# Kernel tuning notes

Measured on AMD Instinct MI355X. Metric: run time of the kernel, lower is better.

## Reference

```python
import jax, jax.numpy as jnp
import numpy as np

BITS = 4
MAXQ = 15            # 2**BITS - 1
PACK = 32 // BITS    # 8 int4 values per int32
GROUPSIZE = 128
M, K, N = 2048, 4096, 4096
G = K // GROUPSIZE


def setup_inputs() -> dict:
    key = jax.random.key(0)
    k1, k2, k3, k4, k5 = jax.random.split(key, 5)
    x = jax.random.normal(k1, (M, K), dtype=jnp.float32)
    qweight = jax.random.randint(k2, (K // PACK, N), 0, 2147483647, dtype=jnp.int32)
    qzeros = jax.random.randint(k3, (G, N // PACK), 0, 2147483647, dtype=jnp.int32)
    scales = jax.random.uniform(k4, (G, N), dtype=jnp.float32) * 0.01
    g_idx = (jnp.arange(K, dtype=jnp.int32) // GROUPSIZE).astype(jnp.int32)
    bias = jax.random.normal(k5, (N,), dtype=jnp.float32)
    return {"x": x, "qweight": qweight, "qzeros": qzeros,
            "scales": scales, "g_idx": g_idx, "bias": bias}


def _dequantize(qweight, qzeros, scales, g_idx):
    shifts = (jnp.arange(PACK, dtype=jnp.int32) * BITS)
    # unpack weights along K: [K//8, N] -> [K//8, 8, N] -> [K, N]
    w_int = ((qweight[:, None, :] >> shifts[None, :, None]) & MAXQ)
    w_int = w_int.reshape(K, N)
    # unpack zeros along N: [G, N//8] -> [G, N//8, 8] -> [G, N]; kernel adds 1
    z_int = ((qzeros[:, :, None] >> shifts[None, None, :]) & MAXQ) + 1
    z_int = z_int.reshape(G, N)
    # group-wise dequant: W[k, n] = (w - zeros[g_idx[k]]) * scales[g_idx[k]]
    W = (w_int - z_int[g_idx]).astype(jnp.float32) * scales[g_idx]
    return W  # [K, N]


def reference(x, qweight, qzeros, scales, g_idx, bias):
    W = _dequantize(qweight, qzeros, scales, g_idx)
    return x @ W + bias  # [M, N]
```

## Files before the change

kernel.cpp:

```cpp
#include <hip/hip_runtime.h>
#include <hip/hip_bf16.h>
#include <stdint.h>

#define M_DIM 2048
#define K_DIM 4096
#define N_DIM 4096

typedef __attribute__((ext_vector_type(8))) short short8;
typedef __attribute__((ext_vector_type(4))) float f32x4;

__device__ __forceinline__ uint32_t bf16pk(float a, float b) {
  uint32_t ua = __float_as_uint(a);
  ua = (ua + 0x7FFFu + ((ua >> 16) & 1u)) >> 16;
  uint32_t ub = __float_as_uint(b);
  ub = (ub + 0x7FFFu + ((ub >> 16) & 1u)) >> 16;
  return ua | (ub << 16);
}

__global__ void __launch_bounds__(256) cvt_x_kernel(const float* __restrict__ x,
                                                    uint32_t* __restrict__ xImg) {
  int bid = blockIdx.x;
  int mt = bid >> 6;
  int kt = bid & 63;
  int tid = threadIdx.x;
  uint32_t* tileOut = xImg + (size_t)(mt * 64 + kt) * 4096;
  const float* xbase = x + (size_t)mt * 128 * K_DIM + kt * 64;
#pragma unroll
  for (int i = 0; i < 4; ++i) {
    int o = i * 256 + tid;
    int m = o >> 3;
    int slot = o & 7;
    int k8 = slot ^ (m & 7);
    const float* src = xbase + (size_t)m * K_DIM + k8 * 8;
    float4 f0 = *(const float4*)(src);
    float4 f1 = *(const float4*)(src + 4);
    uint4 pk;
    pk.x = bf16pk(f0.x, f0.y);
    pk.y = bf16pk(f0.z, f0.w);
    pk.z = bf16pk(f1.x, f1.y);
    pk.w = bf16pk(f1.z, f1.w);
    *(uint4*)(tileOut + (size_t)o * 4) = pk;
  }
}

__global__ void __launch_bounds__(256) deq_w_kernel(const uint32_t* __restrict__ qweight,
                                                    const uint32_t* __restrict__ qzeros,
                                                    const float* __restrict__ scales,
                                                    uint32_t* __restrict__ wImg) {
  __shared__ uint32_t img[4096];
  int bid = blockIdx.x;
  int kt = bid & 63;
  int nt = bid >> 6;
  int tid = threadIdx.x;
  int n = tid & 127;
  int kh = tid >> 7;
  int g = kt >> 1;
  int gn = nt * 128 + n;

  uint32_t zq = qzeros[g * (N_DIM / 8) + (gn >> 3)];
  int z = (int)((zq >> ((gn & 7) * 4)) & 15u) + 1;
  float s = scales[g * N_DIM + gn];

#pragma unroll
  for (int j = 0; j < 4; ++j) {
    int k8 = kh * 4 + j;
    uint32_t q = qweight[(size_t)(kt * 8 + k8) * N_DIM + gn];
    float f[8];
#pragma unroll
    for (int v = 0; v < 8; ++v) {
      int w = (int)((q >> (4 * v)) & 15u);
      f[v] = (float)(w - z) * s;
    }
    uint4 pk;
    pk.x = bf16pk(f[0], f[1]);
    pk.y = bf16pk(f[2], f[3]);
    pk.z = bf16pk(f[4], f[5]);
    pk.w = bf16pk(f[6], f[7]);
    int slot = k8 ^ (n & 7);
    *(uint4*)(&img[(n * 8 + slot) * 4]) = pk;
  }
  __syncthreads();
  uint32_t* tileOut = wImg + (size_t)(nt * 64 + kt) * 4096;
#pragma unroll
  for (int i = 0; i < 4; ++i) {
    int o = i * 256 + tid;
    *(uint4*)(tileOut + (size_t)o * 4) = *(const uint4*)(&img[o * 4]);
  }
}

__global__ void __launch_bounds__(256) gemm_kernel(const uint32_t* __restrict__ xImg,
                                                   const uint32_t* __restrict__ wImg,
                                                   const float* __restrict__ bias,
                                                   float* __restrict__ out) {
  __shared__ uint32_t sA[4096];
  __shared__ uint32_t sB[4096];
  int bid = blockIdx.x;
  int nb = bid & 31;
  int mb = bid >> 5;
  int tid = threadIdx.x;
  int lane = tid & 63;
  int wid = tid >> 6;
  int wr = wid >> 1, wc = wid & 1;
  int lr = lane & 15, lk = lane >> 4;

  f32x4 acc[4][4];
#pragma unroll
  for (int i = 0; i < 4; ++i)
#pragma unroll
    for (int j = 0; j < 4; ++j) acc[i][j] = f32x4{0.f, 0.f, 0.f, 0.f};

  const char* aTile = (const char*)(xImg + (size_t)mb * 64 * 4096);
  const char* bTile = (const char*)(wImg + (size_t)nb * 64 * 4096);

  int swz = (lr & 7) << 4;
  int rowA[4], rowB[4];
#pragma unroll
  for (int i = 0; i < 4; ++i) rowA[i] = (wr * 64 + i * 16 + lr) * 128;
#pragma unroll
  for (int j = 0; j < 4; ++j) rowB[j] = (wc * 64 + j * 16 + lr) * 128;

  for (int kt = 0; kt < 64; ++kt) {
#pragma unroll
    for (int s2 = 0; s2 < 4; ++s2) {
      int c = wid * 4 + s2;
      int off = c * 1024 + lane * 16;
      __builtin_amdgcn_global_load_lds(
          (__attribute__((address_space(1))) void*)(aTile + off),
          (__attribute__((address_space(3))) void*)((char*)sA + c * 1024), 16, 0, 0);
      __builtin_amdgcn_global_load_lds(
          (__attribute__((address_space(1))) void*)(bTile + off),
          (__attribute__((address_space(3))) void*)((char*)sB + c * 1024), 16, 0, 0);
    }
    __syncthreads();
#pragma unroll
    for (int ks = 0; ks < 2; ++ks) {
      int kb = ks * 64 + lk * 16;
      int ko = kb ^ swz;
      short8 af[4], bf[4];
#pragma unroll
      for (int i = 0; i < 4; ++i)
        af[i] = *(const short8*)((const char*)sA + rowA[i] + ko);
#pragma unroll
      for (int j = 0; j < 4; ++j)
        bf[j] = *(const short8*)((const char*)sB + rowB[j] + ko);
#pragma unroll
      for (int i = 0; i < 4; ++i)
#pragma unroll
        for (int j = 0; j < 4; ++j)
          acc[i][j] = __builtin_amdgcn_mfma_f32_16x16x32_bf16(af[i], bf[j], acc[i][j], 0, 0, 0);
    }
    __syncthreads();
    aTile += 16384;
    bTile += 16384;
  }

  int colBase = nb * 128 + wc * 64 + lr;
  int rowBase = mb * 128 + wr * 64 + lk * 4;
#pragma unroll
  for (int j = 0; j < 4; ++j) {
    int col = colBase + j * 16;
    float bj = bias[col];
#pragma unroll
    for (int i = 0; i < 4; ++i) {
      int row = rowBase + i * 16;
#pragma unroll
      for (int r = 0; r < 4; ++r) {
        out[(size_t)(row + r) * N_DIM + col] = acc[i][j][r] + bj;
      }
    }
  }
}

__global__ void fallback_kernel(const float* __restrict__ x, const uint32_t* __restrict__ qweight,
                                const uint32_t* __restrict__ qzeros, const float* __restrict__ scales,
                                const float* __restrict__ bias, float* __restrict__ out) {
  __shared__ float xs[16][17];
  __shared__ float ws[16][17];
  int tx = threadIdx.x, ty = threadIdx.y;
  int col = blockIdx.x * 16 + tx;
  int row = blockIdx.y * 16 + ty;
  float acc = 0.f;
  for (int k0 = 0; k0 < K_DIM; k0 += 16) {
    xs[ty][tx] = x[(size_t)row * K_DIM + k0 + tx];
    int k = k0 + ty;
    int g = k >> 7;
    uint32_t q = qweight[(size_t)(k >> 3) * N_DIM + col];
    int w = (int)((q >> ((k & 7) * 4)) & 15u);
    uint32_t zq = qzeros[g * (N_DIM / 8) + (col >> 3)];
    int z = (int)((zq >> ((col & 7) * 4)) & 15u) + 1;
    ws[ty][tx] = (float)(w - z) * scales[g * N_DIM + col];
    __syncthreads();
#pragma unroll
    for (int kk = 0; kk < 16; ++kk) acc += xs[ty][kk] * ws[kk][tx];
    __syncthreads();
  }
  out[(size_t)row * N_DIM + col] = acc + bias[col];
}

extern "C" void kernel_launch(void* const* d_in, const int* in_sizes, int n_in,
                              void* d_out, int out_size, void* d_ws, size_t ws_size,
                              hipStream_t stream) {
  const float* x = (const float*)d_in[0];
  const uint32_t* qweight = (const uint32_t*)d_in[1];
  const uint32_t* qzeros = (const uint32_t*)d_in[2];
  const float* scales = (const float*)d_in[3];
  const float* bias = (const float*)d_in[5];
  float* out = (float*)d_out;

  const size_t X_IMG_BYTES = (size_t)16 * 64 * 16384;
  const size_t W_IMG_BYTES = (size_t)32 * 64 * 16384;

  if (ws_size >= X_IMG_BYTES + W_IMG_BYTES) {
    uint32_t* xImg = (uint32_t*)d_ws;
    uint32_t* wImg = (uint32_t*)((char*)d_ws + X_IMG_BYTES);
    cvt_x_kernel<<<1024, 256, 0, stream>>>(x, xImg);
    deq_w_kernel<<<2048, 256, 0, stream>>>(qweight, qzeros, scales, wImg);
    gemm_kernel<<<512, 256, 0, stream>>>(xImg, wImg, bias, out);
  } else {
    fallback_kernel<<<dim3(N_DIM / 16, M_DIM / 16), dim3(16, 16), 0, stream>>>(
        x, qweight, qzeros, scales, bias, out);
  }
}
```

Baseline: 97.92 us.

## Restructure GEMM into 128x256 tiles with triple-buffered LDS prefetch pipeline

The GEMM now runs 512-thread blocks, each computing a 128x256 output tile, so every A tile is reused across two N tiles. LDS is triple buffered (three 48 KB stages), and global-to-LDS loads for tile t+2 are interleaved with MFMA phases. Synchronisation uses explicit barriers, vmcnt waits and s_setprio around the MFMA groups. The aim is to hide load latency and cut the redundant A traffic. In exchange, 144 KB of LDS and launch_bounds(512,2) may limit occupancy, and the grid shrinks to 256 blocks.

```diff
diff --git a/kernel.cpp b/kernel.cpp
--- a/kernel.cpp
+++ b/kernel.cpp
@@ -88,20 +88,27 @@
   }
 }
 
-__global__ void __launch_bounds__(256) gemm_kernel(const uint32_t* __restrict__ xImg,
-                                                   const uint32_t* __restrict__ wImg,
-                                                   const float* __restrict__ bias,
-                                                   float* __restrict__ out) {
-  __shared__ uint32_t sA[4096];
-  __shared__ uint32_t sB[4096];
-  int bid = blockIdx.x;
-  int nb = bid & 31;
-  int mb = bid >> 5;
-  int tid = threadIdx.x;
-  int lane = tid & 63;
-  int wid = tid >> 6;
-  int wr = wid >> 1, wc = wid & 1;
-  int lr = lane & 15, lk = lane >> 4;
+__device__ __forceinline__ void glds16(const char* g, char* l) {
+  __builtin_amdgcn_global_load_lds((__attribute__((address_space(1))) void*)g,
+                                   (__attribute__((address_space(3))) void*)l, 16, 0, 0);
+}
+__device__ __forceinline__ void stage16k(const char* src, char* dst, int tid, int wid) {
+  glds16(src + tid * 16,        dst + wid * 1024);
+  glds16(src + 8192 + tid * 16, dst + 8192 + wid * 1024);
+}
+
+__global__ void __launch_bounds__(512, 2) gemm_kernel(const uint32_t* __restrict__ xImg,
+                                                      const uint32_t* __restrict__ wImg,
+                                                      const float* __restrict__ bias,
+                                                      float* __restrict__ out) {
+  __shared__ uint4 ldsv[9216];
+  char* lds = (char*)ldsv;
+  const int tid = threadIdx.x;
+  const int lane = tid & 63, wid = tid >> 6;
+  const int wr = wid >> 2, wc = wid & 3;
+  const int lr = lane & 15, lk = lane >> 4;
+  const int bid = blockIdx.x;
+  const int nbp = bid & 15, mb = bid >> 4;
 
   f32x4 acc[4][4];
 #pragma unroll
@@ -109,53 +116,104 @@
 #pragma unroll
     for (int j = 0; j < 4; ++j) acc[i][j] = f32x4{0.f, 0.f, 0.f, 0.f};
 
-  const char* aTile = (const char*)(xImg + (size_t)mb * 64 * 4096);
-  const char* bTile = (const char*)(wImg + (size_t)nb * 64 * 4096);
-
-  int swz = (lr & 7) << 4;
-  int rowA[4], rowB[4];
-#pragma unroll
-  for (int i = 0; i < 4; ++i) rowA[i] = (wr * 64 + i * 16 + lr) * 128;
-#pragma unroll
-  for (int j = 0; j < 4; ++j) rowB[j] = (wc * 64 + j * 16 + lr) * 128;
-
-  for (int kt = 0; kt < 64; ++kt) {
-#pragma unroll
-    for (int s2 = 0; s2 < 4; ++s2) {
-      int c = wid * 4 + s2;
-      int off = c * 1024 + lane * 16;
-      __builtin_amdgcn_global_load_lds(
-          (__attribute__((address_space(1))) void*)(aTile + off),
-          (__attribute__((address_space(3))) void*)((char*)sA + c * 1024), 16, 0, 0);
-      __builtin_amdgcn_global_load_lds(
-          (__attribute__((address_space(1))) void*)(bTile + off),
-          (__attribute__((address_space(3))) void*)((char*)sB + c * 1024), 16, 0, 0);
+  const char* aT  = (const char*)xImg + (size_t)mb * (64 * 16384);
+  const char* bT0 = (const char*)wImg + (size_t)(2 * nbp) * (64 * 16384);
+  const char* bT1 = bT0 + (size_t)(64 * 16384);
+
+  const int swz = (lr & 7) << 4;
+  int aOff[4];
+#pragma unroll
+  for (int i = 0; i < 4; ++i) aOff[i] = (wr * 64 + i * 16 + lr) * 128;
+  const int bBase = 16384 + (wc >> 1) * 16384 + ((wc & 1) * 64 + lr) * 128;
+  const int kOff0 = (lk * 16) ^ swz;
+  const int kOff1 = (64 + lk * 16) ^ swz;
+
+  stage16k(aT,           lds + 0,             tid, wid);
+  stage16k(bT0,          lds + 16384,         tid, wid);
+  stage16k(bT1,          lds + 32768,         tid, wid);
+  stage16k(aT + 16384,   lds + 49152,         tid, wid);
+  stage16k(bT0 + 16384,  lds + 49152 + 16384, tid, wid);
+  stage16k(bT1 + 16384,  lds + 49152 + 32768, tid, wid);
+  asm volatile("s_waitcnt vmcnt(6)" ::: "memory");
+  __builtin_amdgcn_sched_barrier(0);
+  __builtin_amdgcn_s_barrier();
+
+  int c = 0;
+  for (int t = 0; t < 64; ++t) {
+    char* buf = lds + c * 49152;
+    const int bn = (c == 0) ? 2 : c - 1;
+    char* nbuf = lds + bn * 49152;
+    const size_t toff = (size_t)((t + 2) & 63) * 16384;
+
+    short8 af[4][2], bf0, bf1;
+
+#pragma unroll
+    for (int i = 0; i < 4; ++i) {
+      af[i][0] = *(const short8*)(buf + aOff[i] + kOff0);
+      af[i][1] = *(const short8*)(buf + aOff[i] + kOff1);
     }
-    __syncthreads();
-#pragma unroll
-    for (int ks = 0; ks < 2; ++ks) {
-      int kb = ks * 64 + lk * 16;
-      int ko = kb ^ swz;
-      short8 af[4], bf[4];
-#pragma unroll
-      for (int i = 0; i < 4; ++i)
-        af[i] = *(const short8*)((const char*)sA + rowA[i] + ko);
-#pragma unroll
-      for (int j = 0; j < 4; ++j)
-        bf[j] = *(const short8*)((const char*)sB + rowB[j] + ko);
-#pragma unroll
-      for (int i = 0; i < 4; ++i)
-#pragma unroll
-        for (int j = 0; j < 4; ++j)
-          acc[i][j] = __builtin_amdgcn_mfma_f32_16x16x32_bf16(af[i], bf[j], acc[i][j], 0, 0, 0);
-    }
-    __syncthreads();
-    aTile += 16384;
-    bTile += 16384;
-  }
-
-  int colBase = nb * 128 + wc * 64 + lr;
-  int rowBase = mb * 128 + wr * 64 + lk * 4;
+    bf0 = *(const short8*)(buf + bBase + 0 * 2048 + kOff0);
+    bf1 = *(const short8*)(buf + bBase + 0 * 2048 + kOff1);
+    stage16k(aT + toff, nbuf, tid, wid);
+    __builtin_amdgcn_s_barrier();
+    __builtin_amdgcn_s_setprio(1);
+#pragma unroll
+    for (int i = 0; i < 4; ++i)
+      acc[i][0] = __builtin_amdgcn_mfma_f32_16x16x32_bf16(af[i][0], bf0, acc[i][0], 0, 0, 0);
+#pragma unroll
+    for (int i = 0; i < 4; ++i)
+      acc[i][0] = __builtin_amdgcn_mfma_f32_16x16x32_bf16(af[i][1], bf1, acc[i][0], 0, 0, 0);
+    __builtin_amdgcn_s_setprio(0);
+    __builtin_amdgcn_s_barrier();
+
+    bf0 = *(const short8*)(buf + bBase + 1 * 2048 + kOff0);
+    bf1 = *(const short8*)(buf + bBase + 1 * 2048 + kOff1);
+    stage16k(bT0 + toff, nbuf + 16384, tid, wid);
+    __builtin_amdgcn_s_barrier();
+    __builtin_amdgcn_s_setprio(1);
+#pragma unroll
+    for (int i = 0; i < 4; ++i)
+      acc[i][1] = __builtin_amdgcn_mfma_f32_16x16x32_bf16(af[i][0], bf0, acc[i][1], 0, 0, 0);
+#pragma unroll
+    for (int i = 0; i < 4; ++i)
+      acc[i][1] = __builtin_amdgcn_mfma_f32_16x16x32_bf16(af[i][1], bf1, acc[i][1], 0, 0, 0);
+    __builtin_amdgcn_s_setprio(0);
+    __builtin_amdgcn_s_barrier();
+
+    bf0 = *(const short8*)(buf + bBase + 2 * 2048 + kOff0);
+    bf1 = *(const short8*)(buf + bBase + 2 * 2048 + kOff1);
+    stage16k(bT1 + toff, nbuf + 32768, tid, wid);
+    __builtin_amdgcn_s_barrier();
+    __builtin_amdgcn_s_setprio(1);
+#pragma unroll
+    for (int i = 0; i < 4; ++i)
+      acc[i][2] = __builtin_amdgcn_mfma_f32_16x16x32_bf16(af[i][0], bf0, acc[i][2], 0, 0, 0);
+#pragma unroll
+    for (int i = 0; i < 4; ++i)
+      acc[i][2] = __builtin_amdgcn_mfma_f32_16x16x32_bf16(af[i][1], bf1, acc[i][2], 0, 0, 0);
+    __builtin_amdgcn_s_setprio(0);
+    __builtin_amdgcn_s_barrier();
+
+    bf0 = *(const short8*)(buf + bBase + 3 * 2048 + kOff0);
+    bf1 = *(const short8*)(buf + bBase + 3 * 2048 + kOff1);
+    __builtin_amdgcn_s_barrier();
+    __builtin_amdgcn_s_setprio(1);
+#pragma unroll
+    for (int i = 0; i < 4; ++i)
+      acc[i][3] = __builtin_amdgcn_mfma_f32_16x16x32_bf16(af[i][0], bf0, acc[i][3], 0, 0, 0);
+#pragma unroll
+    for (int i = 0; i < 4; ++i)
+      acc[i][3] = __builtin_amdgcn_mfma_f32_16x16x32_bf16(af[i][1], bf1, acc[i][3], 0, 0, 0);
+    __builtin_amdgcn_s_setprio(0);
+    asm volatile("s_waitcnt vmcnt(6)" ::: "memory");
+    __builtin_amdgcn_sched_barrier(0);
+    __builtin_amdgcn_s_barrier();
+
+    c = (c == 2) ? 0 : c + 1;
+  }
+
+  const int colBase = nbp * 256 + wc * 64 + lr;
+  const int rowBase = mb * 128 + wr * 64 + lk * 4;
 #pragma unroll
   for (int j = 0; j < 4; ++j) {
     int col = colBase + j * 16;
@@ -215,7 +273,7 @@
     uint32_t* wImg = (uint32_t*)((char*)d_ws + X_IMG_BYTES);
     cvt_x_kernel<<<1024, 256, 0, stream>>>(x, xImg);
     deq_w_kernel<<<2048, 256, 0, stream>>>(qweight, qzeros, scales, wImg);
-    gemm_kernel<<<512, 256, 0, stream>>>(xImg, wImg, bias, out);
+    gemm_kernel<<<256, 512, 0, stream>>>(xImg, wImg, bias, out);
   } else {
     fallback_kernel<<<dim3(N_DIM / 16, M_DIM / 16), dim3(16, 16), 0, stream>>>(
         x, qweight, qzeros, scales, bias, out);
```

Result: faster. 87.35 us (-10.8%).
